# Performance work log

Measured on AMD Instinct MI355X. Metric: run time of the kernel, lower is better.

## Reference

```python
import jax, jax.numpy as jnp
import numpy as np
import math

E = 100
V = 3
DK = 100
B = 8192
S = 100
T = 10


def setup_inputs() -> dict:
    key = jax.random.key(0)
    ks = jax.random.split(key, 11)
    bound = 1.0 / math.sqrt(E)  # nn.Linear default init range
    def lin(k):
        k1, k2 = jax.random.split(k)
        w = jax.random.uniform(k1, (E, E), jnp.float32, -bound, bound)
        b = jax.random.uniform(k2, (E,), jnp.float32, -bound, bound)
        return w, b
    fc1_w, fc1_b = lin(ks[0])
    fc2_w, fc2_b = lin(ks[1])
    fc3_w, fc3_b = lin(ks[2])
    fc4_w, fc4_b = lin(ks[3])
    vk = jax.random.uniform(ks[4], (V, E), jnp.float32)  # torch.rand
    x = jax.random.normal(ks[5], (B, S, E), jnp.float32)
    tag_embedding = jax.random.normal(ks[6], (B, T, E), jnp.float32)
    return {
        "x": x, "tag_embedding": tag_embedding, "vk": vk,
        "fc1_w": fc1_w, "fc1_b": fc1_b, "fc2_w": fc2_w, "fc2_b": fc2_b,
        "fc3_w": fc3_w, "fc3_b": fc3_b, "fc4_w": fc4_w, "fc4_b": fc4_b,
    }


def reference(x, tag_embedding, vk, fc1_w, fc1_b, fc2_w, fc2_b, fc3_w, fc3_b, fc4_w, fc4_b):
    scale = 1.0 / math.sqrt(DK)
    pad = jnp.float32(-(2.0 ** 32) + 1.0)

    # Stage 1: user behaviors attend over virtual kernels
    of1 = x @ fc1_w.T + fc1_b                      # [B,S,E]
    of2 = vk @ fc2_w.T + fc2_b                     # [V,E]
    m1 = jnp.einsum('bse,ve->bsv', of1, of2) * scale  # [B,S,V]
    sign = jnp.sign(jnp.sum(jnp.abs(x), axis=2))[:, :, None]  # [B,S,1]
    m1 = jnp.where(sign == 0, pad, m1)             # mask zero-padded behaviors
    sm1 = jax.nn.softmax(m1, axis=1)               # softmax over S (dim=1, as in torch)
    ws1 = jnp.einsum('bsv,bse->bve', sm1, of1)     # [B,V,E]

    # Stage 2: tag attends over virtual-kernel summaries
    of3 = vk @ fc3_w.T + fc3_b                     # [V,E]
    of4 = tag_embedding @ fc4_w.T + fc4_b          # [B,T,E]
    m2 = jnp.einsum('bte,ve->btv', of4, of3) * scale  # [B,T,V]
    sm2 = jax.nn.softmax(m2, axis=1)               # softmax over T (dim=1, as in torch)
    user_emb = jnp.einsum('btv,bve->bte', sm2, ws1)  # [B,T,E]

    return jnp.sum(user_emb * tag_embedding, axis=2)  # [B,T]
```

## Files before the change

kernel.cpp:

```cpp
#include <hip/hip_runtime.h>
#include <math.h>

#define E 100
#define V 3
#define S 100
#define T 10
#define NB 8192
#define SCALE 0.1f
#define PADV  (-4294967295.0f)
#define XP 102

#define WS_H  0
#define WS_G  304
#define WS_B1 608
#define WS_C1 708
#define WS_C2 712


__global__ __launch_bounds__(256) void prep_kernel(const float* __restrict__ vk,
        const float* __restrict__ fc1w, const float* __restrict__ fc1b,
        const float* __restrict__ fc2w, const float* __restrict__ fc2b,
        const float* __restrict__ fc3w, const float* __restrict__ fc3b,
        const float* __restrict__ fc4w, const float* __restrict__ fc4b,
        float* __restrict__ ws)
{
    __shared__ __align__(16) float wsm[E * E];
    __shared__ __align__(16) float ofs[V * E];
    const int t   = threadIdx.x;
    const int blk = blockIdx.x;
    const float* WA = blk ? fc4w : fc1w;
    const float* WB = blk ? fc3w : fc2w;
    const float* bB = blk ? fc3b : fc2b;
    const float* bA = blk ? fc4b : fc1b;

    for (int i = t; i < E * E / 4; i += 256)
        *(float4*)(&wsm[4 * i]) = *(const float4*)(WA + 4 * i);

    for (int o = t; o < V * E; o += 256) {
        int v = o / E, e = o % E;
        const float* vr = vk + v * E;
        const float* wr = WB + e * E;
        float acc = bB[e];
        for (int k = 0; k < E; k += 4) {
            float4 a = *(const float4*)(vr + k);
            float4 w = *(const float4*)(wr + k);
            acc += a.x * w.x + a.y * w.y + a.z * w.z + a.w * w.w;
        }
        ofs[o] = acc;
    }
    __syncthreads();

    for (int o = t; o < V * E; o += 256) {
        int v = o / E, k = o % E;
        float acc = 0.f;
        for (int e = 0; e < E; ++e) acc += ofs[v * E + e] * wsm[e * E + k];
        ws[(blk ? WS_G : WS_H) + o] = acc * SCALE;
    }
    if (t < V) {
        float acc = 0.f;
        for (int e = 0; e < E; ++e) acc += bA[e] * ofs[t * E + e];
        ws[(blk ? WS_C2 : WS_C1) + t] = acc * SCALE;
    }
    if (blk == 0 && t < E) ws[WS_B1 + t] = fc1b[t];
}

__global__ __launch_bounds__(256) void mvke_main(const float* __restrict__ x,
        const float* __restrict__ tag, const float* __restrict__ fc1w,
        const float* __restrict__ ws, float* __restrict__ out)
{
    __shared__ __align__(16) float xs[S * XP];
    __shared__ __align__(16) float tg[T * E];
    __shared__ __align__(16) float Hs[V * E];
    __shared__ __align__(16) float Gs[V * E];
    __shared__ __align__(16) float b1s[E];
    __shared__ float cs[8];
    __shared__ __align__(16) float m1s[V * S];
    __shared__ __align__(16) float sm1s[V * S];
    __shared__ __align__(16) float ys[V * E];
    __shared__ __align__(16) float ws1s[V * E];
    __shared__ float m2s[T * V];
    __shared__ float sm2s[T * V];
    __shared__ float p3[32];

    const int t = threadIdx.x;
    const int b = blockIdx.x;
    const float* xb = x   + (size_t)b * (S * E);
    const float* tb = tag + (size_t)b * (T * E);

    for (int i = t; i < (S * E + T * E) / 4; i += 256) {
        if (i < S * E / 4) {
            int s = i / 25, kk = (i % 25) * 4;
            float4 v = *(const float4*)(xb + s * E + kk);
            float* d = &xs[s * XP + kk];
            *(float2*)(d)     = make_float2(v.x, v.y);
            *(float2*)(d + 2) = make_float2(v.z, v.w);
        } else {
            int j = i - S * E / 4;
            *(float4*)(&tg[4 * j]) = *(const float4*)(tb + 4 * j);
        }
    }
    if (t < 75)        *(float4*)(&Hs[4 * t])         = *(const float4*)(ws + WS_H  + 4 * t);
    else if (t < 150)  *(float4*)(&Gs[4 * (t - 75)])  = *(const float4*)(ws + WS_G  + 4 * (t - 75));
    else if (t < 175)  *(float4*)(&b1s[4 * (t - 150)]) = *(const float4*)(ws + WS_B1 + 4 * (t - 150));
    else if (t < 183)  cs[t - 175] = ws[WS_C1 + (t - 175)];
    __syncthreads();

    if (t < S) {
        const float* xr = &xs[t * XP];
        float a0 = cs[0], a1 = cs[1], a2 = cs[2], ra = 0.f;
        #pragma unroll 2
        for (int k = 0; k < E; k += 2) {
            float2 xv = *(const float2*)(xr + k);
            float2 h0 = *(const float2*)(&Hs[k]);
            float2 h1 = *(const float2*)(&Hs[E + k]);
            float2 h2 = *(const float2*)(&Hs[2 * E + k]);
            a0 += xv.x * h0.x + xv.y * h0.y;
            a1 += xv.x * h1.x + xv.y * h1.y;
            a2 += xv.x * h2.x + xv.y * h2.y;
            ra += fabsf(xv.x) + fabsf(xv.y);
        }
        bool z = (ra == 0.f);
        m1s[t]         = z ? PADV : a0;
        m1s[S + t]     = z ? PADV : a1;
        m1s[2 * S + t] = z ? PADV : a2;
    } else if (t >= 128 && t < 128 + T * V) {
        int o = t - 128, tt = o / V, v = o % V;
        const float* tr = &tg[tt * E];
        const float* gr = &Gs[v * E];
        float acc = cs[4 + v];
        #pragma unroll 2
        for (int k = 0; k < E; k += 4) {
            float4 a = *(const float4*)(tr + k);
            float4 g = *(const float4*)(gr + k);
            acc += a.x * g.x + a.y * g.y + a.z * g.z + a.w * g.w;
        }
        m2s[o] = acc;
    }
    __syncthreads();

    {
        int wv = t >> 6, lane = t & 63;
        if (wv < V) {
            float x1 = m1s[wv * S + lane];
            float x2 = (lane + 64 < S) ? m1s[wv * S + lane + 64] : -INFINITY;
            float mx = fmaxf(x1, x2);
            for (int d = 32; d > 0; d >>= 1) mx = fmaxf(mx, __shfl_xor(mx, d));
            float e1 = __expf(x1 - mx);
            float e2 = (lane + 64 < S) ? __expf(x2 - mx) : 0.f;
            float sm = e1 + e2;
            for (int d = 32; d > 0; d >>= 1) sm += __shfl_xor(sm, d);
            float inv = 1.f / sm;
            sm1s[wv * S + lane] = e1 * inv;
            if (lane + 64 < S) sm1s[wv * S + lane + 64] = e2 * inv;
        } else if (lane < V) {
            float mm[T];
            float mx = -INFINITY;
            for (int tt = 0; tt < T; ++tt) { mm[tt] = m2s[tt * V + lane]; mx = fmaxf(mx, mm[tt]); }
            float ee[T];
            float sum = 0.f;
            for (int tt = 0; tt < T; ++tt) { ee[tt] = __expf(mm[tt] - mx); sum += ee[tt]; }
            float inv = 1.f / sum;
            for (int tt = 0; tt < T; ++tt) sm2s[tt * V + lane] = ee[tt] * inv;
        }
    }
    __syncthreads();

    for (int o = t; o < V * E; o += 256) {
        int v = o / E, k = o % E;
        const float* smr = &sm1s[v * S];
        const float* xc  = &xs[k];
        float acc = 0.f;
        #pragma unroll 4
        for (int s = 0; s < S; ++s) acc += smr[s] * xc[s * XP];
        ys[o] = acc;
    }
    __syncthreads();

    for (int o = t; o < V * E; o += 256) {
        int v = o / E, e = o % E;
        const float* wr = fc1w + e * E;
        const float* yr = &ys[v * E];
        float acc = b1s[e];
        #pragma unroll 5
        for (int k = 0; k < E; k += 4) {
            float4 w  = *(const float4*)(wr + k);
            float4 yv = *(const float4*)(&yr[k]);
            acc += w.x * yv.x + w.y * yv.y + w.z * yv.z + w.w * yv.w;
        }
        ws1s[o] = acc;
    }
    __syncthreads();

    if (t < T * V) {
        int tt = t / V, v = t % V;
        const float* wr = &ws1s[v * E];
        const float* tr = &tg[tt * E];
        float acc = 0.f;
        #pragma unroll 5
        for (int k = 0; k < E; k += 4) {
            float4 w = *(const float4*)(wr + k);
            float4 a = *(const float4*)(tr + k);
            acc += w.x * a.x + w.y * a.y + w.z * a.z + w.w * a.w;
        }
        p3[t] = sm2s[t] * acc;
    }
    __syncthreads();
    if (t < T)
        out[(size_t)b * T + t] = p3[t * V] + p3[t * V + 1] + p3[t * V + 2];
}

extern "C" void kernel_launch(void* const* d_in, const int* in_sizes, int n_in,
                              void* d_out, int out_size, void* d_ws, size_t ws_size,
                              hipStream_t stream) {
    const float* x    = (const float*)d_in[0];
    const float* tag  = (const float*)d_in[1];
    const float* vk   = (const float*)d_in[2];
    const float* fc1w = (const float*)d_in[3];
    const float* fc1b = (const float*)d_in[4];
    const float* fc2w = (const float*)d_in[5];
    const float* fc2b = (const float*)d_in[6];
    const float* fc3w = (const float*)d_in[7];
    const float* fc3b = (const float*)d_in[8];
    const float* fc4w = (const float*)d_in[9];
    const float* fc4b = (const float*)d_in[10];
    float* out = (float*)d_out;
    float* ws  = (float*)d_ws;

    hipLaunchKernelGGL(prep_kernel, dim3(2), dim3(256), 0, stream,
                       vk, fc1w, fc1b, fc2w, fc2b, fc3w, fc3b, fc4w, fc4b, ws);
    hipLaunchKernelGGL(mvke_main, dim3(NB), dim3(256), 0, stream,
                       x, tag, fc1w, ws, out);
}
```

Before: 611.8 us.

## Read x directly from global memory instead of staging it in LDS

Removes the 40KB shared-memory copy of x and has the mask/score pass and the weighted-sum pass read x straight from global memory, relying on L2/L1 for the second read. Shared memory use drops, so launch bounds now ask for 8 blocks per SM. Loops are widened to float4 and two accumulators. The cost is a second global pass over x, whose loads in the sm1·x loop are strided by row and may be poorly coalesced or miss cache.

```diff
diff --git a/kernel.cpp b/kernel.cpp
--- a/kernel.cpp
+++ b/kernel.cpp
@@ -8,7 +8,6 @@
 #define NB 8192
 #define SCALE 0.1f
 #define PADV  (-4294967295.0f)
-#define XP 102
 
 #define WS_H  0
 #define WS_G  304
@@ -64,11 +63,10 @@
     if (blk == 0 && t < E) ws[WS_B1 + t] = fc1b[t];
 }
 
-__global__ __launch_bounds__(256) void mvke_main(const float* __restrict__ x,
+__global__ __launch_bounds__(256, 8) void mvke_main(const float* __restrict__ x,
         const float* __restrict__ tag, const float* __restrict__ fc1w,
         const float* __restrict__ ws, float* __restrict__ out)
 {
-    __shared__ __align__(16) float xs[S * XP];
     __shared__ __align__(16) float tg[T * E];
     __shared__ __align__(16) float Hs[V * E];
     __shared__ __align__(16) float Gs[V * E];
@@ -87,37 +85,27 @@
     const float* xb = x   + (size_t)b * (S * E);
     const float* tb = tag + (size_t)b * (T * E);
 
-    for (int i = t; i < (S * E + T * E) / 4; i += 256) {
-        if (i < S * E / 4) {
-            int s = i / 25, kk = (i % 25) * 4;
-            float4 v = *(const float4*)(xb + s * E + kk);
-            float* d = &xs[s * XP + kk];
-            *(float2*)(d)     = make_float2(v.x, v.y);
-            *(float2*)(d + 2) = make_float2(v.z, v.w);
-        } else {
-            int j = i - S * E / 4;
-            *(float4*)(&tg[4 * j]) = *(const float4*)(tb + 4 * j);
-        }
-    }
-    if (t < 75)        *(float4*)(&Hs[4 * t])         = *(const float4*)(ws + WS_H  + 4 * t);
-    else if (t < 150)  *(float4*)(&Gs[4 * (t - 75)])  = *(const float4*)(ws + WS_G  + 4 * (t - 75));
+    for (int i = t; i < T * E / 4; i += 256)
+        *(float4*)(&tg[4 * i]) = *(const float4*)(tb + 4 * i);
+    if (t < 75)        *(float4*)(&Hs[4 * t])          = *(const float4*)(ws + WS_H  + 4 * t);
+    else if (t < 150)  *(float4*)(&Gs[4 * (t - 75)])   = *(const float4*)(ws + WS_G  + 4 * (t - 75));
     else if (t < 175)  *(float4*)(&b1s[4 * (t - 150)]) = *(const float4*)(ws + WS_B1 + 4 * (t - 150));
     else if (t < 183)  cs[t - 175] = ws[WS_C1 + (t - 175)];
     __syncthreads();
 
     if (t < S) {
-        const float* xr = &xs[t * XP];
+        const float* xr = xb + t * E;
         float a0 = cs[0], a1 = cs[1], a2 = cs[2], ra = 0.f;
-        #pragma unroll 2
-        for (int k = 0; k < E; k += 2) {
-            float2 xv = *(const float2*)(xr + k);
-            float2 h0 = *(const float2*)(&Hs[k]);
-            float2 h1 = *(const float2*)(&Hs[E + k]);
-            float2 h2 = *(const float2*)(&Hs[2 * E + k]);
-            a0 += xv.x * h0.x + xv.y * h0.y;
-            a1 += xv.x * h1.x + xv.y * h1.y;
-            a2 += xv.x * h2.x + xv.y * h2.y;
-            ra += fabsf(xv.x) + fabsf(xv.y);
+        #pragma unroll 5
+        for (int k = 0; k < E; k += 4) {
+            float4 xv = *(const float4*)(xr + k);
+            float4 h0 = *(const float4*)(&Hs[k]);
+            float4 h1 = *(const float4*)(&Hs[E + k]);
+            float4 h2 = *(const float4*)(&Hs[2 * E + k]);
+            a0 += xv.x * h0.x + xv.y * h0.y + xv.z * h0.z + xv.w * h0.w;
+            a1 += xv.x * h1.x + xv.y * h1.y + xv.z * h1.z + xv.w * h1.w;
+            a2 += xv.x * h2.x + xv.y * h2.y + xv.z * h2.z + xv.w * h2.w;
+            ra += fabsf(xv.x) + fabsf(xv.y) + fabsf(xv.z) + fabsf(xv.w);
         }
         bool z = (ra == 0.f);
         m1s[t]         = z ? PADV : a0;
@@ -128,7 +116,7 @@
         const float* tr = &tg[tt * E];
         const float* gr = &Gs[v * E];
         float acc = cs[4 + v];
-        #pragma unroll 2
+        #pragma unroll 5
         for (int k = 0; k < E; k += 4) {
             float4 a = *(const float4*)(tr + k);
             float4 g = *(const float4*)(gr + k);
@@ -168,11 +156,14 @@
     for (int o = t; o < V * E; o += 256) {
         int v = o / E, k = o % E;
         const float* smr = &sm1s[v * S];
-        const float* xc  = &xs[k];
-        float acc = 0.f;
+        const float* xc  = xb + k;
+        float a0 = 0.f, a1 = 0.f;
         #pragma unroll 4
-        for (int s = 0; s < S; ++s) acc += smr[s] * xc[s * XP];
-        ys[o] = acc;
+        for (int s = 0; s < S; s += 2) {
+            a0 += smr[s]     * xc[s * E];
+            a1 += smr[s + 1] * xc[(s + 1) * E];
+        }
+        ys[o] = a0 + a1;
     }
     __syncthreads();
 
```

Result: slower. 664.8 us (+8.7%).
